# Kernel optimization log

Measured on AMD Instinct MI355X. Metric: run time of the kernel, lower is better.

Reference implementation:

```python
import jax, jax.numpy as jnp
import numpy as np


def setup_inputs() -> dict:
    key = jax.random.key(0)
    k_x, k_w1, k_w2 = jax.random.split(key, 3)
    B, N, F, H = 32, 1024, 512, 2048
    x = jax.random.normal(k_x, (B, N, F), dtype=jnp.float32)
    # first: orthogonal-ish init (Gaussian is fine as a stand-in for correctness testing)
    W1 = jax.random.normal(k_w1, (H, F), dtype=jnp.float32) / np.sqrt(F)
    b1 = jnp.zeros((H,), dtype=jnp.float32)
    # second: normal(std=0.01)
    W2 = jax.random.normal(k_w2, (F, H), dtype=jnp.float32) * 0.01
    b2 = jnp.zeros((F,), dtype=jnp.float32)
    return {"x": x, "W1": W1, "b1": b1, "W2": W2, "b2": b2, "dim": 1}


def reference(x, W1, b1, W2, b2, dim):
    # Move the target feature axis (1 + dim) to last position.
    x = jnp.moveaxis(x, 1 + dim, -1)  # [B, N, F]
    srt = jnp.argsort(x, axis=-1)     # argsort indices
    inv = jnp.argsort(srt, axis=-1)   # inverse permutation
    # torch: x.scatter(-1, argsort, x) -> out[argsort[i]] = x[i] == gather by inverse
    xs = jnp.take_along_axis(x, inv, axis=-1)
    # 2-layer MLP with skip
    h = jax.nn.relu(jnp.einsum('bnf,hf->bnh', xs, W1) + b1)
    y = jnp.einsum('bnh,fh->bnf', h, W2) + b2 + xs
    # torch: y.scatter(-1, inverse, y) -> out[inverse[i]] = y[i] == gather by argsort
    out = jnp.take_along_axis(y, srt, axis=-1)
    return jnp.moveaxis(out, -1, 1 + dim)
```

## Files before the change

kernel.cpp:

```cpp
#include <hip/hip_runtime.h>
#include <hip/hip_bf16.h>

typedef __hip_bfloat16 bf16;
typedef __attribute__((ext_vector_type(8))) short bf16x8;
typedef __attribute__((ext_vector_type(4))) float f32x4;

#define ASYNC_CP16(gsrc, ldst)                                                              \
  __builtin_amdgcn_global_load_lds(                                                         \
      (const __attribute__((address_space(1))) unsigned int*)(gsrc),                        \
      (__attribute__((address_space(3))) unsigned int*)(ldst), 16, 0, 0)

#define BB 32
#define NN 1024
#define FF 512
#define HH 2048
#define M_ROWS (BB * NN)

__global__ __launch_bounds__(256) void cvt_pair(const float* __restrict__ a, bf16* __restrict__ da,
                                                const float* __restrict__ b, bf16* __restrict__ db,
                                                int n) {
  int i = blockIdx.x * 256 + threadIdx.x;
  if (i < n) {
    da[i] = __float2bfloat16(a[i]);
    db[i] = __float2bfloat16(b[i]);
  }
}

template <int IMM>
__device__ __forceinline__ unsigned long long swz64(unsigned long long k) {
  int lo = __builtin_amdgcn_ds_swizzle((int)(unsigned)k, IMM);
  int hi = __builtin_amdgcn_ds_swizzle((int)(unsigned)(k >> 32), IMM);
  return (((unsigned long long)(unsigned)hi) << 32) | (unsigned)lo;
}

__global__ __launch_bounds__(256) void sort_rows_wave(const float* __restrict__ x,
                                                      unsigned* __restrict__ xs_pack,
                                                      unsigned* __restrict__ srt_pack) {
  __shared__ __align__(16) unsigned short scatx[4 * FF];
  const int t = threadIdx.x;
  const int lane = t & 63;
  const int w = t >> 6;
  const size_t row = (size_t)blockIdx.x * 4 + w;
  const float* xr = x + row * FF;

  float4 v0 = *(const float4*)(xr + lane * 8);
  float4 v1 = *(const float4*)(xr + lane * 8 + 4);
  float vals[8] = {v0.x, v0.y, v0.z, v0.w, v1.x, v1.y, v1.z, v1.w};

  unsigned long long key[8];
#pragma unroll
  for (int r = 0; r < 8; r++) {
    unsigned u = __float_as_uint(vals[r]);
    unsigned s = u ^ ((unsigned)((int)u >> 31) | 0x80000000u);
    key[r] = ((unsigned long long)s << 32) | (unsigned)(lane * 8 + r);
  }

#pragma unroll
  for (int k = 2; k <= 512; k <<= 1) {
#pragma unroll
    for (int j = k >> 1; j > 0; j >>= 1) {
      if (j >= 8) {
        const int d = j >> 3;
        unsigned long long o[8];
#pragma unroll
        for (int r = 0; r < 8; r++) {
          if (d == 1)       o[r] = swz64<0x041F>(key[r]);
          else if (d == 2)  o[r] = swz64<0x081F>(key[r]);
          else if (d == 4)  o[r] = swz64<0x101F>(key[r]);
          else if (d == 8)  o[r] = swz64<0x201F>(key[r]);
          else if (d == 16) o[r] = swz64<0x401F>(key[r]);
          else              o[r] = __shfl_xor(key[r], 32, 64);
        }
        bool asc = (((lane * 8) & k) == 0);
        bool lower = ((lane & d) == 0);
        bool keep = (asc == lower);
#pragma unroll
        for (int r = 0; r < 8; r++) {
          bool mine = key[r] < o[r];
          key[r] = (mine == keep) ? key[r] : o[r];
        }
      } else {
#pragma unroll
        for (int r = 0; r < 8; r++) {
          if ((r & j) == 0) {
            const int a = r, b = r | j;
            bool asc = (((lane * 8 + a) & k) == 0);
            unsigned long long ka = key[a], kb = key[b];
            bool sw = ((ka > kb) == asc);
            key[a] = sw ? kb : ka;
            key[b] = sw ? ka : kb;
          }
        }
      }
    }
  }

  const int base = w * FF;
  unsigned j8[8];
#pragma unroll
  for (int r = 0; r < 8; r++) {
    j8[r] = (unsigned)key[r] & 0xFFFFu;
    __hip_bfloat16 hb = __float2bfloat16(vals[r]);
    scatx[base + j8[r]] = *(unsigned short*)&hb;
  }

  uint4 so;
  so.x = j8[0] | (j8[1] << 16);
  so.y = j8[2] | (j8[3] << 16);
  so.z = j8[4] | (j8[5] << 16);
  so.w = j8[6] | (j8[7] << 16);
  *(uint4*)(srt_pack + row * 256 + lane * 4) = so;

  __syncthreads();
  uint4 xo = *(const uint4*)&scatx[base + lane * 8];
  *(uint4*)(xs_pack + row * 256 + lane * 4) = xo;
}

template <int RELU, int ADDX, int K, int N>
__global__ __launch_bounds__(512, 2) void gemm8p(const bf16* __restrict__ A,
                                                 const bf16* __restrict__ Bw,
                                                 const float* __restrict__ bias,
                                                 const bf16* __restrict__ xs_add,
                                                 bf16* __restrict__ C) {
  __shared__ __align__(16) bf16 S[65536];
  const int t = threadIdx.x;
  const int lane = t & 63, wave = t >> 6;
  const int waveM = wave >> 2, waveN = wave & 3;

  constexpr int GY = N / 256;
  static_assert((M_ROWS / 256) % 8 == 0, "x-chunking assumes 16 x per XCD");
  const int g = (int)blockIdx.x;
  const int q = g >> 3;
  const size_t mBase = (size_t)((g & 7) * ((M_ROWS / 256) / 8) + q / GY) * 256;
  const size_t nBase = (size_t)(q % GY) * 256;

  const int srow = t >> 2;
  const int sclog = (t & 3) ^ ((t >> 3) & 3);
  const bf16* Asrc0 = A + (mBase + srow) * (size_t)K + sclog * 8;
  const bf16* Bsrc0 = Bw + (nBase + srow) * (size_t)K + sclog * 8;
  const int sdA = wave * 512;
  const int sdB = 32768 + wave * 512;

  const int fr = lane & 15;
  const int swz8 = ((lane >> 4) ^ ((lane >> 1) & 3)) * 8;
  const int aRd = (waveM * 128 + fr) * 32 + swz8;
  const int bRd = 32768 + (waveN * 64 + fr) * 32 + swz8;

#define STAGE_A(tt, ks)                                           \
  do {                                                            \
    const int rb_ = (((tt) & 1) * 2 + (ks)) * 8192 + sdA;         \
    const bf16* g_ = Asrc0 + (size_t)(tt) * 64 + (ks) * 32;       \
    ASYNC_CP16(g_, &S[rb_]);                                      \
    ASYNC_CP16(g_ + (size_t)128 * K, &S[rb_ + 4096]);             \
  } while (0)
#define STAGE_B(tt, ks)                                           \
  do {                                                            \
    const int rb_ = (((tt) & 1) * 2 + (ks)) * 8192 + sdB;         \
    const bf16* g_ = Bsrc0 + (size_t)(tt) * 64 + (ks) * 32;       \
    ASYNC_CP16(g_, &S[rb_]);                                      \
    ASYNC_CP16(g_ + (size_t)128 * K, &S[rb_ + 4096]);             \
  } while (0)

  f32x4 acc[8][4];
  f32x4 zero = {0.f, 0.f, 0.f, 0.f};
#pragma unroll
  for (int i = 0; i < 8; i++)
#pragma unroll
    for (int j = 0; j < 4; j++) acc[i][j] = zero;

  STAGE_A(0, 0);
  STAGE_B(0, 0);
  STAGE_A(0, 1);
  STAGE_B(0, 1);
  asm volatile("s_waitcnt vmcnt(4)" ::: "memory");
  __builtin_amdgcn_s_barrier();

  const int NT = K / 64;
  for (int kt = 0; kt < NT; ++kt) {
    const int buf = kt & 1;
    const bool pf = (kt + 1 < NT);
    bf16x8 af[4], bq[4];

    {
      const int rg = buf * 16384;
#pragma unroll
      for (int i = 0; i < 4; i++) af[i] = *(const bf16x8*)&S[rg + aRd + i * 512];
#pragma unroll
      for (int n = 0; n < 4; n++) bq[n] = *(const bf16x8*)&S[rg + bRd + n * 512];
      if (pf) {
        STAGE_A(kt + 1, 0);
        STAGE_B(kt + 1, 0);
      }
      __builtin_amdgcn_s_barrier();
      asm volatile("s_waitcnt lgkmcnt(0)" ::: "memory");
      __builtin_amdgcn_sched_barrier(0);
      __builtin_amdgcn_s_setprio(1);
#pragma unroll
      for (int i = 0; i < 4; i++)
#pragma unroll
        for (int n = 0; n < 4; n++)
          acc[i][n] = __builtin_amdgcn_mfma_f32_16x16x32_bf16(af[i], bq[n], acc[i][n], 0, 0, 0);
      __builtin_amdgcn_s_setprio(0);
      __builtin_amdgcn_s_barrier();
    }
    {
      const int rg = buf * 16384;
#pragma unroll
      for (int i = 0; i < 4; i++) af[i] = *(const bf16x8*)&S[rg + aRd + 2048 + i * 512];
      if (pf) {
        STAGE_A(kt + 1, 1);
        STAGE_B(kt + 1, 1);
      }
      __builtin_amdgcn_s_barrier();
      asm volatile("s_waitcnt lgkmcnt(0)" ::: "memory");
      __builtin_amdgcn_sched_barrier(0);
      __builtin_amdgcn_s_setprio(1);
#pragma unroll
      for (int i = 0; i < 4; i++)
#pragma unroll
        for (int n = 0; n < 4; n++)
          acc[4 + i][n] = __builtin_amdgcn_mfma_f32_16x16x32_bf16(af[i], bq[n], acc[4 + i][n], 0, 0, 0);
      __builtin_amdgcn_s_setprio(0);
      if (pf) asm volatile("s_waitcnt vmcnt(8)" ::: "memory");
      else    asm volatile("s_waitcnt vmcnt(0)" ::: "memory");
      __builtin_amdgcn_s_barrier();
    }
    {
      const int rg = buf * 16384 + 8192;
#pragma unroll
      for (int i = 0; i < 4; i++) af[i] = *(const bf16x8*)&S[rg + aRd + i * 512];
#pragma unroll
      for (int n = 0; n < 4; n++) bq[n] = *(const bf16x8*)&S[rg + bRd + n * 512];
      __builtin_amdgcn_s_barrier();
      asm volatile("s_waitcnt lgkmcnt(0)" ::: "memory");
      __builtin_amdgcn_sched_barrier(0);
      __builtin_amdgcn_s_setprio(1);
#pragma unroll
      for (int i = 0; i < 4; i++)
#pragma unroll
        for (int n = 0; n < 4; n++)
          acc[i][n] = __builtin_amdgcn_mfma_f32_16x16x32_bf16(af[i], bq[n], acc[i][n], 0, 0, 0);
      __builtin_amdgcn_s_setprio(0);
      __builtin_amdgcn_s_barrier();
    }
    {
      const int rg = buf * 16384 + 8192;
#pragma unroll
      for (int i = 0; i < 4; i++) af[i] = *(const bf16x8*)&S[rg + aRd + 2048 + i * 512];
      __builtin_amdgcn_s_barrier();
      asm volatile("s_waitcnt lgkmcnt(0)" ::: "memory");
      __builtin_amdgcn_sched_barrier(0);
      __builtin_amdgcn_s_setprio(1);
#pragma unroll
      for (int i = 0; i < 4; i++)
#pragma unroll
        for (int n = 0; n < 4; n++)
          acc[4 + i][n] = __builtin_amdgcn_mfma_f32_16x16x32_bf16(af[i], bq[n], acc[4 + i][n], 0, 0, 0);
      __builtin_amdgcn_s_setprio(0);
      if (pf) asm volatile("s_waitcnt vmcnt(4)" ::: "memory");
      __builtin_amdgcn_s_barrier();
    }
  }
#undef STAGE_A
#undef STAGE_B

  const int cn = lane & 15;
  const int cm = (lane >> 4) * 4;
  float b4[4];
#pragma unroll
  for (int n = 0; n < 4; n++) b4[n] = bias[nBase + waveN * 64 + n * 16 + cn];
#pragma unroll
  for (int mt = 0; mt < 8; mt++) {
#pragma unroll
    for (int n = 0; n < 4; n++) {
      size_t gn = nBase + waveN * 64 + n * 16 + cn;
#pragma unroll
      for (int r = 0; r < 4; r++) {
        size_t gm = mBase + waveM * 128 + mt * 16 + cm + r;
        float v = acc[mt][n][r] + b4[n];
        if (RELU) v = fmaxf(v, 0.f);
        if (ADDX) v += __bfloat162float(xs_add[gm * (size_t)N + gn]);
        C[gm * (size_t)N + gn] = __float2bfloat16(v);
      }
    }
  }
}

__global__ __launch_bounds__(256) void permute_gather(const bf16* __restrict__ zp,
                                                      const unsigned* __restrict__ srt_pack,
                                                      float* __restrict__ out) {
  __shared__ __align__(16) unsigned short zr[4][FF];
  const int t = threadIdx.x;
  const int lane = t & 63;
  const int w = t >> 6;
  const size_t row = (size_t)blockIdx.x * 4 + w;

  *(uint4*)&zr[w][lane * 8] = *(const uint4*)(zp + row * FF + lane * 8);
  uint4 sv = *(const uint4*)(srt_pack + row * 256 + lane * 4);
  __syncthreads();

  unsigned idx[8] = {sv.x & 0xFFFFu, sv.x >> 16, sv.y & 0xFFFFu, sv.y >> 16,
                     sv.z & 0xFFFFu, sv.z >> 16, sv.w & 0xFFFFu, sv.w >> 16};
  float4 o0, o1;
#pragma unroll
  for (int r = 0; r < 8; r++) {
    float zf = __uint_as_float(((unsigned)zr[w][idx[r]]) << 16);
    ((r < 4) ? (&o0.x) : (&o1.x))[r & 3] = zf;
  }
  *(float4*)(out + row * FF + lane * 8) = o0;
  *(float4*)(out + row * FF + lane * 8 + 4) = o1;
}

extern "C" void kernel_launch(void* const* d_in, const int* in_sizes, int n_in,
                              void* d_out, int out_size, void* d_ws, size_t ws_size,
                              hipStream_t stream) {
  const float* x  = (const float*)d_in[0];
  const float* W1 = (const float*)d_in[1];
  const float* b1 = (const float*)d_in[2];
  const float* W2 = (const float*)d_in[3];
  const float* b2 = (const float*)d_in[4];
  float* out = (float*)d_out;

  char* ws = (char*)d_ws;
  unsigned* xs  = (unsigned*)(ws);
  bf16*     xsb = (bf16*)(ws);
  bf16*     z   = (bf16*)(ws);
  unsigned* srt = (unsigned*)(ws + 33554432);
  bf16* h   = (bf16*)(ws + 67108864);
  bf16* W1b = (bf16*)(ws + 201326592);
  bf16* W2b = (bf16*)(ws + 203423744);

  cvt_pair<<<(HH * FF + 255) / 256, 256, 0, stream>>>(W1, W1b, W2, W2b, HH * FF);
  sort_rows_wave<<<M_ROWS / 4, 256, 0, stream>>>(x, xs, srt);
  gemm8p<1, 0, FF, HH><<<(M_ROWS / 256) * (HH / 256), 512, 0, stream>>>(xsb, W1b, b1, nullptr, h);
  gemm8p<0, 1, HH, FF><<<(M_ROWS / 256) * (FF / 256), 512, 0, stream>>>(h, W2b, b2, xsb, z);
  permute_gather<<<M_ROWS / 4, 256, 0, stream>>>(z, srt, out);
}
```

Before: 375.1 us.

## Merge GEMM k-loop into two phases with split lgkmcnt waits

The four barrier-separated MFMA phases per K tile become two phases. Each phase loads both A halves and the B fragment up front and waits on lgkmcnt(4), so the first 16 MFMAs start while the second A half is still arriving from LDS. This halves the number of block barriers per K tile and overlaps LDS reads with matrix math. In exchange it holds extra fragment registers and changes the vmcnt waits on the prefetch stages, which could expose a race if the counts are off.

```diff
diff --git a/kernel.cpp b/kernel.cpp
--- a/kernel.cpp
+++ b/kernel.cpp
@@ -179,83 +179,71 @@
   for (int kt = 0; kt < NT; ++kt) {
     const int buf = kt & 1;
     const bool pf = (kt + 1 < NT);
-    bf16x8 af[4], bq[4];
+    bf16x8 af0[4], af1[4], bq[4];
 
     {
       const int rg = buf * 16384;
 #pragma unroll
-      for (int i = 0; i < 4; i++) af[i] = *(const bf16x8*)&S[rg + aRd + i * 512];
+      for (int i = 0; i < 4; i++) af0[i] = *(const bf16x8*)&S[rg + aRd + i * 512];
 #pragma unroll
       for (int n = 0; n < 4; n++) bq[n] = *(const bf16x8*)&S[rg + bRd + n * 512];
+      __builtin_amdgcn_sched_barrier(0);
+#pragma unroll
+      for (int i = 0; i < 4; i++) af1[i] = *(const bf16x8*)&S[rg + aRd + 2048 + i * 512];
       if (pf) {
         STAGE_A(kt + 1, 0);
         STAGE_B(kt + 1, 0);
       }
       __builtin_amdgcn_s_barrier();
+      asm volatile("s_waitcnt lgkmcnt(4)" ::: "memory");
+      __builtin_amdgcn_sched_barrier(0);
+      __builtin_amdgcn_s_setprio(1);
+#pragma unroll
+      for (int i = 0; i < 4; i++)
+#pragma unroll
+        for (int n = 0; n < 4; n++)
+          acc[i][n] = __builtin_amdgcn_mfma_f32_16x16x32_bf16(af0[i], bq[n], acc[i][n], 0, 0, 0);
       asm volatile("s_waitcnt lgkmcnt(0)" ::: "memory");
       __builtin_amdgcn_sched_barrier(0);
-      __builtin_amdgcn_s_setprio(1);
 #pragma unroll
       for (int i = 0; i < 4; i++)
 #pragma unroll
         for (int n = 0; n < 4; n++)
-          acc[i][n] = __builtin_amdgcn_mfma_f32_16x16x32_bf16(af[i], bq[n], acc[i][n], 0, 0, 0);
+          acc[4 + i][n] = __builtin_amdgcn_mfma_f32_16x16x32_bf16(af1[i], bq[n], acc[4 + i][n], 0, 0, 0);
       __builtin_amdgcn_s_setprio(0);
+      if (pf) asm volatile("s_waitcnt vmcnt(4)" ::: "memory");
+      else    asm volatile("s_waitcnt vmcnt(0)" ::: "memory");
       __builtin_amdgcn_s_barrier();
     }
     {
-      const int rg = buf * 16384;
-#pragma unroll
-      for (int i = 0; i < 4; i++) af[i] = *(const bf16x8*)&S[rg + aRd + 2048 + i * 512];
+      const int rg = buf * 16384 + 8192;
+#pragma unroll
+      for (int i = 0; i < 4; i++) af0[i] = *(const bf16x8*)&S[rg + aRd + i * 512];
+#pragma unroll
+      for (int n = 0; n < 4; n++) bq[n] = *(const bf16x8*)&S[rg + bRd + n * 512];
+      __builtin_amdgcn_sched_barrier(0);
+#pragma unroll
+      for (int i = 0; i < 4; i++) af1[i] = *(const bf16x8*)&S[rg + aRd + 2048 + i * 512];
       if (pf) {
         STAGE_A(kt + 1, 1);
         STAGE_B(kt + 1, 1);
       }
       __builtin_amdgcn_s_barrier();
+      asm volatile("s_waitcnt lgkmcnt(4)" ::: "memory");
+      __builtin_amdgcn_sched_barrier(0);
+      __builtin_amdgcn_s_setprio(1);
+#pragma unroll
+      for (int i = 0; i < 4; i++)
+#pragma unroll
+        for (int n = 0; n < 4; n++)
+          acc[i][n] = __builtin_amdgcn_mfma_f32_16x16x32_bf16(af0[i], bq[n], acc[i][n], 0, 0, 0);
       asm volatile("s_waitcnt lgkmcnt(0)" ::: "memory");
       __builtin_amdgcn_sched_barrier(0);
-      __builtin_amdgcn_s_setprio(1);
 #pragma unroll
       for (int i = 0; i < 4; i++)
 #pragma unroll
         for (int n = 0; n < 4; n++)
-          acc[4 + i][n] = __builtin_amdgcn_mfma_f32_16x16x32_bf16(af[i], bq[n], acc[4 + i][n], 0, 0, 0);
-      __builtin_amdgcn_s_setprio(0);
-      if (pf) asm volatile("s_waitcnt vmcnt(8)" ::: "memory");
-      else    asm volatile("s_waitcnt vmcnt(0)" ::: "memory");
-      __builtin_amdgcn_s_barrier();
-    }
-    {
-      const int rg = buf * 16384 + 8192;
-#pragma unroll
-      for (int i = 0; i < 4; i++) af[i] = *(const bf16x8*)&S[rg + aRd + i * 512];
-#pragma unroll
-      for (int n = 0; n < 4; n++) bq[n] = *(const bf16x8*)&S[rg + bRd + n * 512];
-      __builtin_amdgcn_s_barrier();
-      asm volatile("s_waitcnt lgkmcnt(0)" ::: "memory");
-      __builtin_amdgcn_sched_barrier(0);
-      __builtin_amdgcn_s_setprio(1);
-#pragma unroll
-      for (int i = 0; i < 4; i++)
-#pragma unroll
-        for (int n = 0; n < 4; n++)
-          acc[i][n] = __builtin_amdgcn_mfma_f32_16x16x32_bf16(af[i], bq[n], acc[i][n], 0, 0, 0);
-      __builtin_amdgcn_s_setprio(0);
-      __builtin_amdgcn_s_barrier();
-    }
-    {
-      const int rg = buf * 16384 + 8192;
-#pragma unroll
-      for (int i = 0; i < 4; i++) af[i] = *(const bf16x8*)&S[rg + aRd + 2048 + i * 512];
-      __builtin_amdgcn_s_barrier();
-      asm volatile("s_waitcnt lgkmcnt(0)" ::: "memory");
-      __builtin_amdgcn_sched_barrier(0);
-      __builtin_amdgcn_s_setprio(1);
-#pragma unroll
-      for (int i = 0; i < 4; i++)
-#pragma unroll
-        for (int n = 0; n < 4; n++)
-          acc[4 + i][n] = __builtin_amdgcn_mfma_f32_16x16x32_bf16(af[i], bq[n], acc[4 + i][n], 0, 0, 0);
+          acc[4 + i][n] = __builtin_amdgcn_mfma_f32_16x16x32_bf16(af1[i], bq[n], acc[4 + i][n], 0, 0, 0);
       __builtin_amdgcn_s_setprio(0);
       if (pf) asm volatile("s_waitcnt vmcnt(4)" ::: "memory");
       __builtin_amdgcn_s_barrier();
```

After: 343.3 us. 1.09x faster.
